# Performance work log

Measured on AMD Instinct MI355X. Metric: run time of the kernel, lower is better.

## Reference

```python
import jax, jax.numpy as jnp
import numpy as np

EMBED_DIM = 1024
NUM_HEADS = 16
FFN_DIM = 4096
N_QUBITS = 8
LN_EPS = 1e-5


def _layernorm(x, g, b):
    mu = jnp.mean(x, axis=-1, keepdims=True)
    var = jnp.mean(jnp.square(x - mu), axis=-1, keepdims=True)
    return (x - mu) * jax.lax.rsqrt(var + LN_EPS) * g + b


def setup_inputs() -> dict:
    key = jax.random.key(0)
    ks = jax.random.split(key, 12)
    E, F_, Q = EMBED_DIM, FFN_DIM, N_QUBITS
    s = 1.0 / np.sqrt(E)
    return {
        "x": jax.random.normal(ks[0], (4, 2048, E), dtype=jnp.float32),
        "wq": jax.random.normal(ks[1], (E, E), dtype=jnp.float32) * s,
        "wk": jax.random.normal(ks[2], (E, E), dtype=jnp.float32) * s,
        "wv": jax.random.normal(ks[3], (E, E), dtype=jnp.float32) * s,
        "wo": jax.random.normal(ks[4], (E, E), dtype=jnp.float32) * s,
        "theta": jax.random.normal(ks[5], (Q,), dtype=jnp.float32),
        "w1": jax.random.normal(ks[6], (Q, F_), dtype=jnp.float32) * (1.0 / np.sqrt(Q)),
        "w2": jax.random.normal(ks[7], (F_, E), dtype=jnp.float32) * (1.0 / np.sqrt(F_)),
        "ln1_g": jnp.ones((E,), dtype=jnp.float32),
        "ln1_b": jnp.zeros((E,), dtype=jnp.float32),
        "ln2_g": jnp.ones((E,), dtype=jnp.float32),
        "ln2_b": jnp.zeros((E,), dtype=jnp.float32),
    }


def reference(x, wq, wk, wv, wo, theta, w1, w2, ln1_g, ln1_b, ln2_g, ln2_b):
    B, S, E = x.shape
    H, Dk = NUM_HEADS, E // NUM_HEADS
    # ---- multi-head attention ----
    q = (x @ wq).reshape(B, S, H, Dk).transpose(0, 2, 1, 3)  # [B,H,S,Dk]
    k = (x @ wk).reshape(B, S, H, Dk).transpose(0, 2, 1, 3)
    v = (x @ wv).reshape(B, S, H, Dk).transpose(0, 2, 1, 3)
    scores = jnp.einsum("bhsd,bhtd->bhst", q, k) / np.sqrt(Dk)
    attn = jax.nn.softmax(scores, axis=-1)
    ctx = jnp.einsum("bhst,bhtd->bhsd", attn, v)
    ctx = ctx.transpose(0, 2, 1, 3).reshape(B, S, E)
    attn_out = ctx @ wo
    x1 = _layernorm(x + attn_out, ln1_g, ln1_b)
    # ---- quantum FFN ----
    # Per qubit w: |0> -> RX(x1_w) -> RX(x1_w) -> RX(theta_w); <Z> = cos(2*x1_w + theta_w)
    q_out = jnp.cos(2.0 * x1[..., :N_QUBITS] + theta)  # [B,S,Q]
    ffn_out = jax.nn.relu(q_out @ w1) @ w2  # [B,S,E]
    return _layernorm(x1 + ffn_out, ln2_g, ln2_b)
```

## Files before the change

### kernel.cpp

```cpp
#include <hip/hip_runtime.h>
#include <hip/hip_bf16.h>


typedef __attribute__((ext_vector_type(8))) short bf16x8;
typedef __attribute__((ext_vector_type(16))) float f32x16;
typedef __attribute__((ext_vector_type(4))) unsigned short u16x4;

__device__ __forceinline__ unsigned short f2bf(float f) {
  union { float f; unsigned int u; } v; v.f = f;
  return (unsigned short)((v.u + 0x7FFFu + ((v.u >> 16) & 1u)) >> 16);
}
__device__ __forceinline__ float bf2f(unsigned short h) {
  union { unsigned int u; float f; } v; v.u = ((unsigned int)h) << 16;
  return v.f;
}
__device__ __forceinline__ f32x16 mfma32(bf16x8 a, bf16x8 b, f32x16 c) {
  return __builtin_amdgcn_mfma_f32_32x32x16_bf16(a, b, c, 0, 0, 0);
}
__device__ __forceinline__ void lds_cp16(const void* g, void* l) {
  __builtin_amdgcn_global_load_lds(
      (const __attribute__((address_space(1))) unsigned int*)g,
      (__attribute__((address_space(3))) unsigned int*)l, 16, 0, 0);
}

#define QG_CONV(P, FC0, FC1)                                                  \
  {                                                                           \
    int x0a, x0b, x1a, x1b, x2a, x2b, x3a, x3b;                               \
    asm("v_cvt_pk_bf16_f32 %0, %1, %2" : "=v"(x0a) : "v"(P[0]),  "v"(P[1]));  \
    asm("v_cvt_pk_bf16_f32 %0, %1, %2" : "=v"(x0b) : "v"(P[2]),  "v"(P[3]));  \
    asm("v_cvt_pk_bf16_f32 %0, %1, %2" : "=v"(x1a) : "v"(P[4]),  "v"(P[5]));  \
    asm("v_cvt_pk_bf16_f32 %0, %1, %2" : "=v"(x1b) : "v"(P[6]),  "v"(P[7]));  \
    asm("v_cvt_pk_bf16_f32 %0, %1, %2" : "=v"(x2a) : "v"(P[8]),  "v"(P[9]));  \
    asm("v_cvt_pk_bf16_f32 %0, %1, %2" : "=v"(x2b) : "v"(P[10]), "v"(P[11])); \
    asm("v_cvt_pk_bf16_f32 %0, %1, %2" : "=v"(x3a) : "v"(P[12]), "v"(P[13])); \
    asm("v_cvt_pk_bf16_f32 %0, %1, %2" : "=v"(x3b) : "v"(P[14]), "v"(P[15])); \
    asm("v_permlane32_swap_b32 %0, %1" : "+v"(x0a), "+v"(x1a));               \
    asm("v_permlane32_swap_b32 %0, %1" : "+v"(x0b), "+v"(x1b));               \
    asm("v_permlane32_swap_b32 %0, %1" : "+v"(x2a), "+v"(x3a));               \
    asm("v_permlane32_swap_b32 %0, %1" : "+v"(x2b), "+v"(x3b));               \
    union { int u[4]; bf16x8 v; } f0_, f1_;                                   \
    f0_.u[0] = x0a; f0_.u[1] = x0b; f0_.u[2] = x1a; f0_.u[3] = x1b;           \
    f1_.u[0] = x2a; f1_.u[1] = x2b; f1_.u[2] = x3a; f1_.u[3] = x3b;           \
    FC0 = f0_.v; FC1 = f1_.v;                                                 \
  }

__global__ __launch_bounds__(256) void cast_x_kernel(const float* __restrict__ in,
                                                     unsigned short* __restrict__ out,
                                                     int n4) {
  int i = blockIdx.x * 256 + threadIdx.x;
  if (i >= n4) return;
  float4 v = ((const float4*)in)[i];
  u16x4 o = { f2bf(v.x), f2bf(v.y), f2bf(v.z), f2bf(v.w) };
  ((u16x4*)out)[i] = o;
}

__global__ __launch_bounds__(256) void transpose_cast_kernel(const float* __restrict__ in,
                                                             unsigned short* __restrict__ out,
                                                             int K, int N) {
  __shared__ float tile[32][33];
  const int n0 = blockIdx.x * 32, k0 = blockIdx.y * 32;
  const int tx = threadIdx.x, ty = threadIdx.y;
#pragma unroll
  for (int i = 0; i < 32; i += 8)
    tile[ty + i][tx] = in[(long)(k0 + ty + i) * N + n0 + tx];
  __syncthreads();
#pragma unroll
  for (int i = 0; i < 32; i += 8)
    out[(long)(n0 + ty + i) * K + k0 + tx] = f2bf(tile[tx][ty + i]);
}

__global__ __launch_bounds__(256) void w1t_kernel(const float* __restrict__ w1,
                                                  unsigned short* __restrict__ w1t) {
  const int f = blockIdx.x * 256 + threadIdx.x;
  unsigned short v[8];
#pragma unroll
  for (int q = 0; q < 8; q++) v[q] = f2bf(w1[q * 4096 + f]);
  *(u16x4*)(w1t + f * 8)     = (u16x4){v[0], v[1], v[2], v[3]};
  *(u16x4*)(w1t + f * 8 + 4) = (u16x4){v[4], v[5], v[6], v[7]};
}

__global__ __launch_bounds__(256) void vt_kernel(const unsigned short* __restrict__ qkv,
                                                 unsigned short* __restrict__ vT) {
  __shared__ unsigned short tile[32][34];
  const int t0 = blockIdx.x * 32, d0 = blockIdx.y * 32, bh = blockIdx.z;
  const int b = bh >> 4, h = bh & 15;
  const int tx = threadIdx.x, ty = threadIdx.y;
  const unsigned short* src = qkv + (long)(b * 2048 + t0) * 3072 + 2048 + h * 64 + d0;
#pragma unroll
  for (int i = 0; i < 32; i += 8)
    tile[ty + i][tx] = src[(long)(ty + i) * 3072 + tx];
  __syncthreads();
  unsigned short* dst = vT + ((long)bh * 64 + d0) * 2048 + t0;
#pragma unroll
  for (int i = 0; i < 32; i += 8)
    dst[(long)(ty + i) * 2048 + tx] = tile[tx][ty + i];
}

template<int EPI>
__global__ __launch_bounds__(256) void gemm_bt3(const unsigned short* __restrict__ A,
                                                const unsigned short* __restrict__ BT,
                                                void* __restrict__ Cv,
                                                int M, int N, int K) {
  __shared__ __align__(16) unsigned char smem[2][32768];
  const int tid = threadIdx.x;
  const int l = tid & 63, w = tid >> 6;
  const int l32 = l & 31, h32 = l >> 5;
  const int wrm = (w >> 1) * 64;
  const int wrn = (w & 1) * 64;

  const int nx = gridDim.x;
  const int nwg = nx * gridDim.y;
  const int orig = blockIdx.y * nx + blockIdx.x;
  const int chunk = nwg >> 3;
  const int logical = (orig & 7) * chunk + (orig >> 3);
  const long m0 = (long)(logical / nx) * 128;
  const long n0 = (long)(logical % nx) * 128;

  const unsigned short* gp[8];
  unsigned ldsoff[8];
#pragma unroll
  for (int i = 0; i < 8; i++) {
    const int c = (i & 3) * 256 + tid;
    const int r = c >> 3, k8 = c & 7;
    if (i < 4) {
      gp[i] = A + (m0 + r) * (long)K + (k8 ^ (r & 7)) * 8;
      ldsoff[i] = (unsigned)c * 16;
    } else {
      gp[i] = BT + (n0 + r) * (long)K + (k8 ^ (r & 7)) * 8;
      ldsoff[i] = 16384u + (unsigned)c * 16;
    }
  }

  f32x16 acc[2][2];
#pragma unroll
  for (int mf = 0; mf < 2; mf++)
#pragma unroll
    for (int nf = 0; nf < 2; nf++)
#pragma unroll
      for (int e = 0; e < 16; e++) acc[mf][nf][e] = 0.f;

  const int NT = K >> 6;
#define STAGE(bf, t)                                                    \
  do {                                                                  \
    unsigned char* _d = &smem[bf][0];                                   \
    const long _ko = (long)(t) * 64;                                    \
    _Pragma("unroll")                                                   \
    for (int _i = 0; _i < 8; _i++)                                      \
      lds_cp16(gp[_i] + _ko, _d + ldsoff[_i]);                          \
  } while (0)

  STAGE(0, 0);
  int cur = 0;
  for (int t = 0; t < NT; t++) {
    if (t + 1 < NT) {
      STAGE(cur ^ 1, t + 1);
      asm volatile("s_waitcnt vmcnt(8)" ::: "memory");
    } else {
      asm volatile("s_waitcnt vmcnt(0)" ::: "memory");
    }
    __builtin_amdgcn_sched_barrier(0);
    __builtin_amdgcn_s_barrier();
    __builtin_amdgcn_sched_barrier(0);

    const unsigned char* bufA = &smem[cur][0];
    const unsigned char* bufB = &smem[cur][16384];
    bf16x8 af[2][4], bfr[2][4];
#pragma unroll
    for (int mf = 0; mf < 2; mf++) {
      const int r = wrm + mf * 32 + l32;
#pragma unroll
      for (int ks = 0; ks < 4; ks++)
        af[mf][ks] = *(const bf16x8*)(bufA + r * 128 + (((ks * 2 + h32) ^ (r & 7)) * 16));
    }
#pragma unroll
    for (int nf = 0; nf < 2; nf++) {
      const int r = wrn + nf * 32 + l32;
#pragma unroll
      for (int ks = 0; ks < 4; ks++)
        bfr[nf][ks] = *(const bf16x8*)(bufB + r * 128 + (((ks * 2 + h32) ^ (r & 7)) * 16));
    }
    __builtin_amdgcn_s_setprio(1);
#pragma unroll
    for (int ks = 0; ks < 4; ks++)
#pragma unroll
      for (int mf = 0; mf < 2; mf++)
#pragma unroll
        for (int nf = 0; nf < 2; nf++)
          acc[mf][nf] = mfma32(af[mf][ks], bfr[nf][ks], acc[mf][nf]);
    __builtin_amdgcn_s_setprio(0);
    __builtin_amdgcn_sched_barrier(0);
    __builtin_amdgcn_s_barrier();
    cur ^= 1;
  }
#undef STAGE

#pragma unroll
  for (int mf = 0; mf < 2; mf++)
#pragma unroll
    for (int nf = 0; nf < 2; nf++) {
      const long c0 = n0 + wrn + nf * 32 + l32;
#pragma unroll
      for (int reg = 0; reg < 16; reg++) {
        const long r0 = m0 + wrm + mf * 32 + (reg & 3) + 8 * (reg >> 2) + 4 * h32;
        if (EPI == 0) ((float*)Cv)[r0 * (long)N + c0] = acc[mf][nf][reg];
        else ((unsigned short*)Cv)[r0 * (long)N + c0] = f2bf(acc[mf][nf][reg]);
      }
    }
}

__global__ __launch_bounds__(512) void ffn_fused(const unsigned short* __restrict__ qo,
                                                 const unsigned short* __restrict__ w1t,
                                                 const unsigned short* __restrict__ BT,
                                                 float* __restrict__ Cp0,
                                                 float* __restrict__ Cp1,
                                                 int N, int K) {
  __shared__ __align__(16) unsigned char sm[2 * 16384 + 32768 + 4096];
  unsigned char* lsW = sm + 32768;
  unsigned char* lsQ = sm + 65536;
  const int tid = threadIdx.x;
  const int l = tid & 63, w = tid >> 6;
  const int l32 = l & 31, h32 = l >> 5;
  const int wrm = (w >> 1) * 64;
  const int wrn = (w & 1) * 64;

  const int nx = gridDim.x;
  const int nwg = nx * gridDim.y;
  const int orig = blockIdx.y * nx + blockIdx.x;
  const int chunk = nwg >> 3;
  const int logical = (orig & 7) * chunk + (orig >> 3);
  const long m0 = (long)(logical / nx) * 256;
  const long n0 = (long)(logical % nx) * 128;
  const int kz = blockIdx.z;
  const int NT = (K >> 6) >> 1;
  const int tbase = kz * NT;
  float* C = kz ? Cp1 : Cp0;

  const unsigned short* gpB[2];
  unsigned offB[2];
#pragma unroll
  for (int i = 0; i < 2; i++) {
    const int c = i * 512 + tid;
    const int r = c >> 3, k8 = c & 7;
    gpB[i] = BT + (n0 + r) * (long)K + (long)tbase * 64 + (k8 ^ (r & 7)) * 8;
    offB[i] = (unsigned)c * 16;
  }
  const unsigned short* w1base = w1t + (long)tbase * 64 * 8;

  const bf16x8 z8 = {0, 0, 0, 0, 0, 0, 0, 0};

#define STAGE_B(bf, t)                                                  \
  do {                                                                  \
    unsigned char* _d = sm + (bf) * 16384;                              \
    const long _ko = (long)(t) * 64;                                    \
    lds_cp16(gpB[0] + _ko, _d + offB[0]);                               \
    lds_cp16(gpB[1] + _ko, _d + offB[1]);                               \
  } while (0)
#define STAGE_W1(T)                                                     \
  lds_cp16(w1base + (long)((T) * 64 + l) * 8, lsW + ((unsigned)(T) << 10))

  STAGE_W1(0);
  STAGE_W1(1);
  if (w < 4) lds_cp16(qo + (m0 + w * 64 + l) * 8, lsQ + (unsigned)(w * 64) * 16);
  STAGE_B(0, 0);
  asm volatile("s_waitcnt vmcnt(0)" ::: "memory");
  __builtin_amdgcn_s_barrier();

  bf16x8 qof[2];
#pragma unroll
  for (int mf = 0; mf < 2; mf++)
    qof[mf] = (h32 == 0) ? *(const bf16x8*)(lsQ + (wrm + mf * 32 + l32) * 16) : z8;

  f32x16 zz;
#pragma unroll
  for (int e = 0; e < 16; e++) zz[e] = 0.f;
  f32x16 acc[2][2];
#pragma unroll
  for (int mf = 0; mf < 2; mf++)
#pragma unroll
    for (int nf = 0; nf < 2; nf++) acc[mf][nf] = zz;

  int cur = 0;
  for (int t = 0; t < NT; t++) {
    if (t + 2 < NT) {
      STAGE_W1(t + 2);
      STAGE_B(cur ^ 1, t + 1);
      asm volatile("s_waitcnt vmcnt(3)" ::: "memory");
    } else if (t + 1 < NT) {
      STAGE_B(cur ^ 1, t + 1);
      asm volatile("s_waitcnt vmcnt(2)" ::: "memory");
    } else {
      asm volatile("s_waitcnt vmcnt(0)" ::: "memory");
    }
    __builtin_amdgcn_sched_barrier(0);
    __builtin_amdgcn_s_barrier();
    __builtin_amdgcn_sched_barrier(0);

    bf16x8 w1f[2];
#pragma unroll
    for (int tg = 0; tg < 2; tg++)
      w1f[tg] = (h32 == 0)
          ? *(const bf16x8*)(lsW + ((unsigned)t << 10) + (tg * 32 + l32) * 16)
          : z8;

    const unsigned char* bufB = sm + cur * 16384;
    bf16x8 bfr[2][4];
#pragma unroll
    for (int nf = 0; nf < 2; nf++) {
      const int r = wrn + nf * 32 + l32;
#pragma unroll
      for (int ks = 0; ks < 4; ks++)
        bfr[nf][ks] = *(const bf16x8*)(bufB + r * 128 + (((ks * 2 + h32) ^ (r & 7)) * 16));
    }

#pragma unroll
    for (int mf = 0; mf < 2; mf++) {
      __builtin_amdgcn_s_setprio(1);
      f32x16 hC0 = mfma32(w1f[0], qof[mf], zz);
      f32x16 hC1 = mfma32(w1f[1], qof[mf], zz);
      __builtin_amdgcn_s_setprio(0);
#pragma unroll
      for (int e = 0; e < 16; e++) {
        hC0[e] = fmaxf(hC0[e], 0.f);
        hC1[e] = fmaxf(hC1[e], 0.f);
      }
      bf16x8 a0, a1, a2, a3;
      QG_CONV(hC0, a0, a1)
      QG_CONV(hC1, a2, a3)
      __builtin_amdgcn_s_setprio(1);
      acc[mf][0] = mfma32(a0, bfr[0][0], acc[mf][0]);
      acc[mf][0] = mfma32(a1, bfr[0][1], acc[mf][0]);
      acc[mf][0] = mfma32(a2, bfr[0][2], acc[mf][0]);
      acc[mf][0] = mfma32(a3, bfr[0][3], acc[mf][0]);
      acc[mf][1] = mfma32(a0, bfr[1][0], acc[mf][1]);
      acc[mf][1] = mfma32(a1, bfr[1][1], acc[mf][1]);
      acc[mf][1] = mfma32(a2, bfr[1][2], acc[mf][1]);
      acc[mf][1] = mfma32(a3, bfr[1][3], acc[mf][1]);
      __builtin_amdgcn_s_setprio(0);
    }
    __builtin_amdgcn_sched_barrier(0);
    __builtin_amdgcn_s_barrier();
    cur ^= 1;
  }
#undef STAGE_B
#undef STAGE_W1

#pragma unroll
  for (int mf = 0; mf < 2; mf++)
#pragma unroll
    for (int nf = 0; nf < 2; nf++) {
      const long c0 = n0 + wrn + nf * 32 + l32;
#pragma unroll
      for (int reg = 0; reg < 16; reg++) {
        const long r0 = m0 + wrm + mf * 32 + (reg & 3) + 8 * (reg >> 2) + 4 * h32;
        C[r0 * (long)N + c0] = acc[mf][nf][reg];
      }
    }
}

#define QG_BLOCK(P, LIP, FC0, FC1)                                            \
  {                                                                           \
    _Pragma("unroll")                                                         \
    for (int e = 0; e < 16; e++)                                              \
      asm("v_exp_f32 %0, %1" : "=v"(P[e]) : "v"(P[e]));                       \
    float s_ = 0.f;                                                           \
    _Pragma("unroll")                                                         \
    for (int e = 0; e < 16; e++) s_ += P[e];                                  \
    LIP += s_;                                                                \
    QG_CONV(P, FC0, FC1)                                                      \
  }

__global__ __launch_bounds__(256) void attn_kernel(const unsigned short* __restrict__ qkv,
                                                   const unsigned short* __restrict__ vT,
                                                   unsigned short* __restrict__ ctx) {
  __shared__ __align__(16) unsigned short lsK[64][72];
  __shared__ __align__(16) unsigned short lsV[64][72];

  const int tid = threadIdx.x;
  const int l = tid & 63, w = tid >> 6;
  const int l32 = l & 31, h32 = l >> 5;

  const int orig = blockIdx.x;
  const int logical = (orig & 7) * 64 + (orig >> 3);
  const int s0 = (logical & 7) * 256;
  const int bh = logical >> 3;
  const int b = bh >> 4, hh = bh & 15;

  const float QSC = 0.18033688f;
  const unsigned short* qg_base = qkv + (long)(b * 2048 + s0 + w * 64) * 3072 + hh * 64;
  bf16x8 qb0[4], qb1[4];
#pragma unroll
  for (int kc = 0; kc < 4; kc++) {
    bf16x8 t0v = *(const bf16x8*)(qg_base + (long)l32 * 3072 + kc * 16 + h32 * 8);
    bf16x8 t1v = *(const bf16x8*)(qg_base + (long)(32 + l32) * 3072 + kc * 16 + h32 * 8);
#pragma unroll
    for (int j = 0; j < 8; j++) {
      t0v[j] = (short)f2bf(bf2f((unsigned short)t0v[j]) * QSC);
      t1v[j] = (short)f2bf(bf2f((unsigned short)t1v[j]) * QSC);
    }
    qb0[kc] = t0v;
    qb1[kc] = t1v;
  }

  f32x16 oacc00, oacc01, oacc10, oacc11;
#pragma unroll
  for (int e = 0; e < 16; e++) {
    oacc00[e] = 0.f; oacc01[e] = 0.f; oacc10[e] = 0.f; oacc11[e] = 0.f;
  }
  float lip0 = 0.f, lip1 = 0.f;

  const int tr = tid >> 2;
  const int tc = (tid & 3) * 16;
  const unsigned short* kbase = qkv + (long)(b * 2048) * 3072 + 1024 + hh * 64;
  const unsigned short* vbase = vT + (long)bh * 64 * 2048;

  bf16x8 k0 = *(const bf16x8*)(kbase + (long)tr * 3072 + tc);
  bf16x8 k1 = *(const bf16x8*)(kbase + (long)tr * 3072 + tc + 8);
  bf16x8 v0 = *(const bf16x8*)(vbase + (long)tr * 2048 + tc);
  bf16x8 v1 = *(const bf16x8*)(vbase + (long)tr * 2048 + tc + 8);

  for (int t0 = 0; t0 < 2048; t0 += 64) {
    __syncthreads();
    *(bf16x8*)&lsK[tr][tc]     = k0;
    *(bf16x8*)&lsK[tr][tc + 8] = k1;
    *(bf16x8*)&lsV[tr][tc]     = v0;
    *(bf16x8*)&lsV[tr][tc + 8] = v1;
    __syncthreads();
    if (t0 + 64 < 2048) {
      k0 = *(const bf16x8*)(kbase + (long)(t0 + 64 + tr) * 3072 + tc);
      k1 = *(const bf16x8*)(kbase + (long)(t0 + 64 + tr) * 3072 + tc + 8);
      v0 = *(const bf16x8*)(vbase + (long)tr * 2048 + t0 + 64 + tc);
      v1 = *(const bf16x8*)(vbase + (long)tr * 2048 + t0 + 64 + tc + 8);
    }

#pragma unroll
    for (int tg = 0; tg < 2; tg++) {
      bf16x8 kb[4];
#pragma unroll
      for (int kc = 0; kc < 4; kc++)
        kb[kc] = *(const bf16x8*)&lsK[tg * 32 + l32][kc * 16 + h32 * 8];

      f32x16 p0, p1;
#pragma unroll
      for (int e = 0; e < 16; e++) { p0[e] = 0.f; p1[e] = 0.f; }
      __builtin_amdgcn_s_setprio(1);
#pragma unroll
      for (int kc = 0; kc < 4; kc++) {
        p0 = mfma32(kb[kc], qb0[kc], p0);
        p1 = mfma32(kb[kc], qb1[kc], p1);
      }
      __builtin_amdgcn_s_setprio(0);

      bf16x8 fA0, fA1, fB0, fB1;
      QG_BLOCK(p0, lip0, fA0, fA1)
      QG_BLOCK(p1, lip1, fB0, fB1)

      bf16x8 v00 = *(const bf16x8*)&lsV[l32][tg * 32 + h32 * 8];
      bf16x8 v01 = *(const bf16x8*)&lsV[l32][tg * 32 + 16 + h32 * 8];
      bf16x8 v10 = *(const bf16x8*)&lsV[32 + l32][tg * 32 + h32 * 8];
      bf16x8 v11 = *(const bf16x8*)&lsV[32 + l32][tg * 32 + 16 + h32 * 8];

      __builtin_amdgcn_s_setprio(1);
      oacc00 = mfma32(fA0, v00, oacc00);
      oacc00 = mfma32(fA1, v01, oacc00);
      oacc01 = mfma32(fA0, v10, oacc01);
      oacc01 = mfma32(fA1, v11, oacc01);
      oacc10 = mfma32(fB0, v00, oacc10);
      oacc10 = mfma32(fB1, v01, oacc10);
      oacc11 = mfma32(fB0, v10, oacc11);
      oacc11 = mfma32(fB1, v11, oacc11);
      __builtin_amdgcn_s_setprio(0);
    }
  }

  const float li0 = lip0 + __shfl_xor(lip0, 32);
  const float li1 = lip1 + __shfl_xor(lip1, 32);
  const float inv0 = 1.f / li0;
  const float inv1 = 1.f / li1;
  const long qrow0 = (long)(b * 2048 + s0 + w * 64);
  const int dcol = hh * 64 + l32;
#define STORE_QG(OA, OB, INV, QOFF)                                           \
  _Pragma("unroll")                                                           \
  for (int reg = 0; reg < 16; reg++) {                                        \
    const int rq = (reg & 3) + 8 * (reg >> 2) + 4 * h32;                      \
    const float iv = __shfl(INV, rq);                                         \
    const long q = qrow0 + (QOFF) + rq;                                       \
    ctx[q * 1024 + dcol]      = f2bf(OA[reg] * iv);                           \
    ctx[q * 1024 + dcol + 32] = f2bf(OB[reg] * iv);                           \
  }
  STORE_QG(oacc00, oacc01, inv0, 0)
  STORE_QG(oacc10, oacc11, inv1, 32)
#undef STORE_QG
}

template<bool QO, bool THREE>
__global__ __launch_bounds__(256) void ln_kernel(const float* __restrict__ ra,
                                                 const float* __restrict__ rb,
                                                 const float* __restrict__ rc,
                                                 const float* __restrict__ g,
                                                 const float* __restrict__ bb,
                                                 float* __restrict__ out,
                                                 unsigned short* __restrict__ qo,
                                                 const float* __restrict__ theta) {
  const int row = blockIdx.x;
  const int tid = threadIdx.x;
  const long base = (long)row * 1024 + tid * 4;
  float4 a = *(const float4*)(ra + base);
  float4 bv = *(const float4*)(rb + base);
  float4 r;
  r.x = a.x + bv.x; r.y = a.y + bv.y; r.z = a.z + bv.z; r.w = a.w + bv.w;
  if constexpr (THREE) {
    float4 c = *(const float4*)(rc + base);
    r.x += c.x; r.y += c.y; r.z += c.z; r.w += c.w;
  }
  float s  = r.x + r.y + r.z + r.w;
  float ss = r.x * r.x + r.y * r.y + r.z * r.z + r.w * r.w;
  for (int off = 32; off; off >>= 1) {
    s  += __shfl_down(s, off);
    ss += __shfl_down(ss, off);
  }
  __shared__ float red[4][2];
  const int wv = tid >> 6;
  if ((tid & 63) == 0) { red[wv][0] = s; red[wv][1] = ss; }
  __syncthreads();
  s  = red[0][0] + red[1][0] + red[2][0] + red[3][0];
  ss = red[0][1] + red[1][1] + red[2][1] + red[3][1];
  const float mu  = s * (1.f / 1024.f);
  const float var = ss * (1.f / 1024.f) - mu * mu;
  const float rsv = rsqrtf(var + 1e-5f);
  float4 gv  = *(const float4*)(g + tid * 4);
  float4 bbv = *(const float4*)(bb + tid * 4);
  float4 y;
  y.x = (r.x - mu) * rsv * gv.x + bbv.x;
  y.y = (r.y - mu) * rsv * gv.y + bbv.y;
  y.z = (r.z - mu) * rsv * gv.z + bbv.z;
  y.w = (r.w - mu) * rsv * gv.w + bbv.w;
  *(float4*)(out + base) = y;
  if constexpr (QO) {
    if (tid < 2) {
      float yv[4] = {y.x, y.y, y.z, y.w};
      u16x4 o;
#pragma unroll
      for (int c = 0; c < 4; c++)
        o[c] = f2bf(__cosf(2.f * yv[c] + theta[tid * 4 + c]));
      *(u16x4*)(qo + (long)row * 8 + tid * 4) = o;
    }
  }
}

extern "C" void kernel_launch(void* const* d_in, const int* in_sizes, int n_in,
                              void* d_out, int out_size, void* d_ws, size_t ws_size,
                              hipStream_t stream) {
  const float* x     = (const float*)d_in[0];
  const float* wq    = (const float*)d_in[1];
  const float* wk    = (const float*)d_in[2];
  const float* wv    = (const float*)d_in[3];
  const float* wo    = (const float*)d_in[4];
  const float* theta = (const float*)d_in[5];
  const float* w1    = (const float*)d_in[6];
  const float* w2    = (const float*)d_in[7];
  const float* g1    = (const float*)d_in[8];
  const float* b1    = (const float*)d_in[9];
  const float* g2    = (const float*)d_in[10];
  const float* b2    = (const float*)d_in[11];
  float* out = (float*)d_out;
  char* ws = (char*)d_ws;

  const long MB = 1 << 20;
  unsigned short* xb    = (unsigned short*)(ws);
  unsigned short* wqkvT = (unsigned short*)(ws + 16 * MB);
  unsigned short* woT   = (unsigned short*)(ws + 22 * MB);
  unsigned short* w2T   = (unsigned short*)(ws + 24 * MB);
  float*          x1    = (float*)(ws + 32 * MB);
  float*          fbuf  = (float*)(ws + 64 * MB);
  unsigned short* qkv   = (unsigned short*)(ws + 96 * MB);
  float*          fbuf2 = (float*)(ws + 96 * MB);
  unsigned short* vTb   = (unsigned short*)(ws + 144 * MB);
  unsigned short* qob   = (unsigned short*)(ws + 160 * MB);
  unsigned short* w1tb  = (unsigned short*)(ws + 160 * MB + 128 * 1024);
  unsigned short* ctx   = xb;

  cast_x_kernel<<<8192, 256, 0, stream>>>(x, xb, 8192 * 1024 / 4);
  dim3 tb(32, 8);
  transpose_cast_kernel<<<dim3(32, 32), tb, 0, stream>>>(wq, wqkvT, 1024, 1024);
  transpose_cast_kernel<<<dim3(32, 32), tb, 0, stream>>>(wk, wqkvT + 1024 * 1024, 1024, 1024);
  transpose_cast_kernel<<<dim3(32, 32), tb, 0, stream>>>(wv, wqkvT + 2048 * 1024, 1024, 1024);
  transpose_cast_kernel<<<dim3(32, 32), tb, 0, stream>>>(wo, woT, 1024, 1024);
  transpose_cast_kernel<<<dim3(32, 128), tb, 0, stream>>>(w2, w2T, 4096, 1024);
  w1t_kernel<<<16, 256, 0, stream>>>(w1, w1tb);

  gemm_bt3<1><<<dim3(24, 64), 256, 0, stream>>>(xb, wqkvT, qkv, 8192, 3072, 1024);

  vt_kernel<<<dim3(64, 2, 64), tb, 0, stream>>>(qkv, vTb);

  attn_kernel<<<512, 256, 0, stream>>>(qkv, vTb, ctx);

  gemm_bt3<0><<<dim3(8, 64), 256, 0, stream>>>(ctx, woT, fbuf, 8192, 1024, 1024);

  ln_kernel<true, false><<<8192, 256, 0, stream>>>(x, fbuf, nullptr, g1, b1, x1, qob, theta);

  ffn_fused<<<dim3(8, 32, 2), 512, 0, stream>>>(qob, w1tb, w2T, fbuf, fbuf2, 1024, 4096);

  ln_kernel<false, true><<<8192, 256, 0, stream>>>(x1, fbuf, fbuf2, g2, b2, out, nullptr, nullptr);
}
```

Baseline: 345.5 us.

## Software-pipeline FFN hidden MFMAs and compute softmax row sums via MFMA

In the quantum-FFN GEMM the first-layer MFMA for the next fragment is issued ahead, alongside the second-layer MFMAs of the current one. This hides the ReLU and bf16 conversion latency behind matrix work. In attention, the per-lane scalar accumulation of exp values is replaced by extra MFMAs against a ones vector, so the row sums arrive already laid out like the output accumulators. That removes the VALU reduction and shuffles but adds four MFMAs per tile, two more accumulator registers, and row sums built from the bf16-rounded probabilities.

```diff
diff --git a/kernel.cpp b/kernel.cpp
--- a/kernel.cpp
+++ b/kernel.cpp
@@ -279,6 +279,14 @@
 #pragma unroll
     for (int nf = 0; nf < 2; nf++) acc[mf][nf] = zz;
 
+  f32x16 hP0, hP1;
+  {
+    bf16x8 wf0 = (h32 == 0) ? *(const bf16x8*)(lsW + (0 + l32) * 16) : z8;
+    bf16x8 wf1 = (h32 == 0) ? *(const bf16x8*)(lsW + (32 + l32) * 16) : z8;
+    hP0 = mfma32(wf0, qof[0], zz);
+    hP1 = mfma32(wf1, qof[0], zz);
+  }
+
   int cur = 0;
   for (int t = 0; t < NT; t++) {
     if (t + 2 < NT) {
@@ -295,13 +303,14 @@
     __builtin_amdgcn_s_barrier();
     __builtin_amdgcn_sched_barrier(0);
 
-    bf16x8 w1f[2];
-#pragma unroll
-    for (int tg = 0; tg < 2; tg++)
-      w1f[tg] = (h32 == 0)
-          ? *(const bf16x8*)(lsW + ((unsigned)t << 10) + (tg * 32 + l32) * 16)
-          : z8;
-
+    bf16x8 w1ft[2], w1fn[2];
+#pragma unroll
+    for (int tg = 0; tg < 2; tg++) {
+      w1ft[tg] = (h32 == 0)
+          ? *(const bf16x8*)(lsW + ((unsigned)t << 10) + (tg * 32 + l32) * 16) : z8;
+      w1fn[tg] = (h32 == 0 && t + 1 < NT)
+          ? *(const bf16x8*)(lsW + ((unsigned)(t + 1) << 10) + (tg * 32 + l32) * 16) : z8;
+    }
     const unsigned char* bufB = sm + cur * 16384;
     bf16x8 bfr[2][4];
 #pragma unroll
@@ -313,30 +322,47 @@
     }
 
 #pragma unroll
-    for (int mf = 0; mf < 2; mf++) {
-      __builtin_amdgcn_s_setprio(1);
-      f32x16 hC0 = mfma32(w1f[0], qof[mf], zz);
-      f32x16 hC1 = mfma32(w1f[1], qof[mf], zz);
-      __builtin_amdgcn_s_setprio(0);
-#pragma unroll
-      for (int e = 0; e < 16; e++) {
-        hC0[e] = fmaxf(hC0[e], 0.f);
-        hC1[e] = fmaxf(hC1[e], 0.f);
-      }
-      bf16x8 a0, a1, a2, a3;
-      QG_CONV(hC0, a0, a1)
-      QG_CONV(hC1, a2, a3)
-      __builtin_amdgcn_s_setprio(1);
-      acc[mf][0] = mfma32(a0, bfr[0][0], acc[mf][0]);
-      acc[mf][0] = mfma32(a1, bfr[0][1], acc[mf][0]);
-      acc[mf][0] = mfma32(a2, bfr[0][2], acc[mf][0]);
-      acc[mf][0] = mfma32(a3, bfr[0][3], acc[mf][0]);
-      acc[mf][1] = mfma32(a0, bfr[1][0], acc[mf][1]);
-      acc[mf][1] = mfma32(a1, bfr[1][1], acc[mf][1]);
-      acc[mf][1] = mfma32(a2, bfr[1][2], acc[mf][1]);
-      acc[mf][1] = mfma32(a3, bfr[1][3], acc[mf][1]);
-      __builtin_amdgcn_s_setprio(0);
-    }
+    for (int e = 0; e < 16; e++) {
+      hP0[e] = fmaxf(hP0[e], 0.f);
+      hP1[e] = fmaxf(hP1[e], 0.f);
+    }
+    bf16x8 a0, a1, a2, a3;
+    QG_CONV(hP0, a0, a1)
+    QG_CONV(hP1, a2, a3)
+    __builtin_amdgcn_s_setprio(1);
+    f32x16 hQ0 = mfma32(w1ft[0], qof[1], zz);
+    f32x16 hQ1 = mfma32(w1ft[1], qof[1], zz);
+    acc[0][0] = mfma32(a0, bfr[0][0], acc[0][0]);
+    acc[0][0] = mfma32(a1, bfr[0][1], acc[0][0]);
+    acc[0][0] = mfma32(a2, bfr[0][2], acc[0][0]);
+    acc[0][0] = mfma32(a3, bfr[0][3], acc[0][0]);
+    acc[0][1] = mfma32(a0, bfr[1][0], acc[0][1]);
+    acc[0][1] = mfma32(a1, bfr[1][1], acc[0][1]);
+    acc[0][1] = mfma32(a2, bfr[1][2], acc[0][1]);
+    acc[0][1] = mfma32(a3, bfr[1][3], acc[0][1]);
+    __builtin_amdgcn_s_setprio(0);
+
+#pragma unroll
+    for (int e = 0; e < 16; e++) {
+      hQ0[e] = fmaxf(hQ0[e], 0.f);
+      hQ1[e] = fmaxf(hQ1[e], 0.f);
+    }
+    bf16x8 b0, b1, b2, b3;
+    QG_CONV(hQ0, b0, b1)
+    QG_CONV(hQ1, b2, b3)
+    __builtin_amdgcn_s_setprio(1);
+    hP0 = mfma32(w1fn[0], qof[0], zz);
+    hP1 = mfma32(w1fn[1], qof[0], zz);
+    acc[1][0] = mfma32(b0, bfr[0][0], acc[1][0]);
+    acc[1][0] = mfma32(b1, bfr[0][1], acc[1][0]);
+    acc[1][0] = mfma32(b2, bfr[0][2], acc[1][0]);
+    acc[1][0] = mfma32(b3, bfr[0][3], acc[1][0]);
+    acc[1][1] = mfma32(b0, bfr[1][0], acc[1][1]);
+    acc[1][1] = mfma32(b1, bfr[1][1], acc[1][1]);
+    acc[1][1] = mfma32(b2, bfr[1][2], acc[1][1]);
+    acc[1][1] = mfma32(b3, bfr[1][3], acc[1][1]);
+    __builtin_amdgcn_s_setprio(0);
+
     __builtin_amdgcn_sched_barrier(0);
     __builtin_amdgcn_s_barrier();
     cur ^= 1;
@@ -357,16 +383,11 @@
     }
 }
 
-#define QG_BLOCK(P, LIP, FC0, FC1)                                            \
+#define QG_EXP(P)                                                             \
   {                                                                           \
     _Pragma("unroll")                                                         \
     for (int e = 0; e < 16; e++)                                              \
       asm("v_exp_f32 %0, %1" : "=v"(P[e]) : "v"(P[e]));                       \
-    float s_ = 0.f;                                                           \
-    _Pragma("unroll")                                                         \
-    for (int e = 0; e < 16; e++) s_ += P[e];                                  \
-    LIP += s_;                                                                \
-    QG_CONV(P, FC0, FC1)                                                      \
   }
 
 __global__ __launch_bounds__(256) void attn_kernel(const unsigned short* __restrict__ qkv,
@@ -401,12 +422,15 @@
     qb1[kc] = t1v;
   }
 
-  f32x16 oacc00, oacc01, oacc10, oacc11;
+  const short one_bf = (short)0x3F80;
+  const bf16x8 ones8 = {one_bf, one_bf, one_bf, one_bf, one_bf, one_bf, one_bf, one_bf};
+
+  f32x16 oacc00, oacc01, oacc10, oacc11, oSum0, oSum1;
 #pragma unroll
   for (int e = 0; e < 16; e++) {
     oacc00[e] = 0.f; oacc01[e] = 0.f; oacc10[e] = 0.f; oacc11[e] = 0.f;
-  }
-  float lip0 = 0.f, lip1 = 0.f;
+    oSum0[e] = 0.f; oSum1[e] = 0.f;
+  }
 
   const int tr = tid >> 2;
   const int tc = (tid & 3) * 16;
@@ -451,8 +475,10 @@
       __builtin_amdgcn_s_setprio(0);
 
       bf16x8 fA0, fA1, fB0, fB1;
-      QG_BLOCK(p0, lip0, fA0, fA1)
-      QG_BLOCK(p1, lip1, fB0, fB1)
+      QG_EXP(p0)
+      QG_CONV(p0, fA0, fA1)
+      QG_EXP(p1)
+      QG_CONV(p1, fB0, fB1)
 
       bf16x8 v00 = *(const bf16x8*)&lsV[l32][tg * 32 + h32 * 8];
       bf16x8 v01 = *(const bf16x8*)&lsV[l32][tg * 32 + 16 + h32 * 8];
@@ -464,31 +490,31 @@
       oacc00 = mfma32(fA1, v01, oacc00);
       oacc01 = mfma32(fA0, v10, oacc01);
       oacc01 = mfma32(fA1, v11, oacc01);
+      oSum0  = mfma32(fA0, ones8, oSum0);
+      oSum0  = mfma32(fA1, ones8, oSum0);
       oacc10 = mfma32(fB0, v00, oacc10);
       oacc10 = mfma32(fB1, v01, oacc10);
       oacc11 = mfma32(fB0, v10, oacc11);
       oacc11 = mfma32(fB1, v11, oacc11);
+      oSum1  = mfma32(fB0, ones8, oSum1);
+      oSum1  = mfma32(fB1, ones8, oSum1);
       __builtin_amdgcn_s_setprio(0);
     }
   }
 
-  const float li0 = lip0 + __shfl_xor(lip0, 32);
-  const float li1 = lip1 + __shfl_xor(lip1, 32);
-  const float inv0 = 1.f / li0;
-  const float inv1 = 1.f / li1;
   const long qrow0 = (long)(b * 2048 + s0 + w * 64);
   const int dcol = hh * 64 + l32;
-#define STORE_QG(OA, OB, INV, QOFF)                                           \
+#define STORE_QG(OA, OB, OS, QOFF)                                            \
   _Pragma("unroll")                                                           \
   for (int reg = 0; reg < 16; reg++) {                                        \
     const int rq = (reg & 3) + 8 * (reg >> 2) + 4 * h32;                      \
-    const float iv = __shfl(INV, rq);                                         \
+    const float iv = 1.f / OS[reg];                                           \
     const long q = qrow0 + (QOFF) + rq;                                       \
     ctx[q * 1024 + dcol]      = f2bf(OA[reg] * iv);                           \
     ctx[q * 1024 + dcol + 32] = f2bf(OB[reg] * iv);                           \
   }
-  STORE_QG(oacc00, oacc01, inv0, 0)
-  STORE_QG(oacc10, oacc11, inv1, 32)
+  STORE_QG(oacc00, oacc01, oSum0, 0)
+  STORE_QG(oacc10, oacc11, oSum1, 32)
 #undef STORE_QG
 }
 
```

Result: slower. 355.2 us (+2.8%).
